# Kernel optimization log

Measured on AMD Instinct MI355X. Metric: run time of the kernel, lower is better.

## Reference

```python
import jax, jax.numpy as jnp
import numpy as np

BATCH = 2048
TEMP = 0.5

def setup_inputs() -> dict:
    key = jax.random.key(0)
    k1, k2 = jax.random.split(key)
    z1 = jax.random.normal(k1, (BATCH, 1024), dtype=jnp.float32)
    z2 = jax.random.normal(k2, (BATCH, 1024), dtype=jnp.float32)
    return {"z1": z1, "z2": z2}

def _l2norm(x, eps=1e-12):
    # matches F.normalize(dim=1): x / max(||x||, eps)
    n = jnp.sqrt(jnp.sum(x * x, axis=1, keepdims=True))
    return x / jnp.maximum(n, eps)

def reference(z1, z2):
    B = z1.shape[0]
    z1n = _l2norm(z1)
    z2n = _l2norm(z2)
    z = jnp.concatenate([z1n, z2n], axis=0)  # [2B, C], unit-norm rows
    # cosine_similarity of unit vectors == dot product -> single GEMM
    S = z @ z.T  # [2B, 2B]
    # positives: S[i, i+B] for i<B and S[i, i-B] for i>=B
    pos_upper = jnp.diagonal(S, offset=B)   # [B]
    pos_lower = jnp.diagonal(S, offset=-B)  # [B]
    positives = jnp.concatenate([pos_upper, pos_lower], axis=0)  # [2B]
    neg_mask = 1.0 - jnp.eye(2 * B, dtype=S.dtype)
    den = jnp.sum(neg_mask * jnp.exp(S / TEMP), axis=1)  # [2B]
    loss = -jnp.mean(positives / TEMP - jnp.log(den))
    return loss
```

## Files before the change

### kernel.cpp

```cpp
#include <hip/hip_runtime.h>
#include <hip/hip_bf16.h>

#define NROW 4096
#define HALFB 2048
#define CDIM 1024
#define INV_T 2.0f
#define NBLK 32
#define NTRI 528
#define NT 8
#define RB 512
#define SCALE_E8M0 122

typedef __attribute__((ext_vector_type(4))) float f32x4;
typedef __attribute__((ext_vector_type(8))) int i32x8;

__device__ __forceinline__ unsigned enc_fp4(float q) {
    const unsigned s = q < 0.f ? 8u : 0u;
    const float a = fabsf(q);
    unsigned m;
    if (a < 1.25f) {
        if (a < 0.25f)      m = 0;
        else if (a < 0.75f) m = 1;
        else                m = 2;
    } else if (a < 2.5f) {
        m = (a < 1.75f) ? 3u : 4u;
    } else {
        if (a < 3.5f)       m = 5;
        else if (a < 5.0f)  m = 6;
        else                m = 7;
    }
    return s | m;
}

__global__ __launch_bounds__(256) void normalize_kernel(
        const float* __restrict__ z1, const float* __restrict__ z2,
        unsigned short* __restrict__ zb4, float* __restrict__ den,
        float* __restrict__ out) {
    const int row = blockIdx.x;
    const int t = threadIdx.x;
    if (row < 16) den[row * 256 + t] = 0.f;
    else if (row == 16 && t == 0) out[0] = 0.f;
    const float* src = (row < HALFB) ? (z1 + (size_t)row * CDIM)
                                     : (z2 + (size_t)(row - HALFB) * CDIM);
    float4 v = ((const float4*)src)[t];
    float ss = v.x * v.x + v.y * v.y + v.z * v.z + v.w * v.w;
    #pragma unroll
    for (int off = 1; off < 64; off <<= 1) ss += __shfl_xor(ss, off);
    __shared__ float wsum[4];
    const int lane = t & 63, wv = t >> 6;
    if (lane == 0) wsum[wv] = ss;
    __syncthreads();
    const float tot = wsum[0] + wsum[1] + wsum[2] + wsum[3];
    const float scale = 32.0f / fmaxf(sqrtf(tot), 1e-12f);
    const unsigned c0 = enc_fp4(v.x * scale);
    const unsigned c1 = enc_fp4(v.y * scale);
    const unsigned c2 = enc_fp4(v.z * scale);
    const unsigned c3 = enc_fp4(v.w * scale);
    zb4[(size_t)row * 256 + t] = (unsigned short)(c0 | (c1 << 4) | (c2 << 8) | (c3 << 12));
}

__global__ __launch_bounds__(256) void gemm_den_kernel(
        const unsigned char* __restrict__ zb4, float* __restrict__ den,
        float* __restrict__ pos) {
    __shared__ __align__(16) unsigned char As[2][128 * 64];
    __shared__ __align__(16) unsigned char Bs[2][128 * 64];

    const int orig = blockIdx.x;
    int swz = (orig & 7) * (NTRI / 8) + (orig >> 3);
    int bi = 0, rem = swz;
    while (rem >= NBLK - bi) { rem -= NBLK - bi; ++bi; }
    const int bj = bi + rem;
    const int i0 = bi * 128, j0 = bj * 128;
    const bool diag = (bi == bj);
    const bool is_pos = (bj == bi + 16);

    const int tid = threadIdx.x;
    const int wave = tid >> 6, lane = tid & 63;
    const int wr = wave >> 1, wc = wave & 1;

    f32x4 acc[4][4];
    #pragma unroll
    for (int m = 0; m < 4; m++)
        #pragma unroll
        for (int n = 0; n < 4; n++) acc[m][n] = (f32x4){0.f, 0.f, 0.f, 0.f};

    const int srow = lane >> 2;
    const int schunk = (lane & 3) ^ ((srow >> 1) & 3);

    const int l15 = lane & 15, ks = lane >> 4;

    auto stage = [&](int buf, int t) {
        const int kb = t * 64;
        #pragma unroll
        for (int c = 0; c < 2; ++c) {
            const int r0 = wave * 32 + c * 16;
            const unsigned char* ga =
                zb4 + (size_t)(i0 + r0 + srow) * RB + kb + schunk * 16;
            __builtin_amdgcn_global_load_lds(
                (const __attribute__((address_space(1))) void*)ga,
                (__attribute__((address_space(3))) void*)(As[buf] + r0 * 64),
                16, 0, 0);
            const unsigned char* gb =
                zb4 + (size_t)(j0 + r0 + srow) * RB + kb + schunk * 16;
            __builtin_amdgcn_global_load_lds(
                (const __attribute__((address_space(1))) void*)gb,
                (__attribute__((address_space(3))) void*)(Bs[buf] + r0 * 64),
                16, 0, 0);
        }
    };

    stage(0, 0);
    asm volatile("s_waitcnt vmcnt(0)" ::: "memory");
    __builtin_amdgcn_s_barrier();

    #pragma unroll
    for (int t = 0; t < NT; ++t) {
        const int buf = t & 1;
        if (t + 1 < NT) stage(buf ^ 1, t + 1);

        i32x8 b[4];
        #pragma unroll
        for (int n = 0; n < 4; ++n) {
            const int r = wc * 64 + n * 16 + l15;
            const int slot = ks ^ ((r >> 1) & 3);
            const int4 w = *(const int4*)(Bs[buf] + r * 64 + slot * 16);
            b[n] = (i32x8){w.x, w.y, w.z, w.w, 0, 0, 0, 0};
        }
        __builtin_amdgcn_s_setprio(1);
        #pragma unroll
        for (int m = 0; m < 4; ++m) {
            const int r = wr * 64 + m * 16 + l15;
            const int slot = ks ^ ((r >> 1) & 3);
            const int4 w = *(const int4*)(As[buf] + r * 64 + slot * 16);
            const i32x8 a = (i32x8){w.x, w.y, w.z, w.w, 0, 0, 0, 0};
            #pragma unroll
            for (int n = 0; n < 4; ++n)
                acc[m][n] = __builtin_amdgcn_mfma_scale_f32_16x16x128_f8f6f4(
                    a, b[n], acc[m][n],
                    4 , 4 ,
                    0, SCALE_E8M0, 0, SCALE_E8M0);
        }
        __builtin_amdgcn_s_setprio(0);
        if (t + 1 < NT) {
            asm volatile("s_waitcnt vmcnt(0)" ::: "memory");
            __builtin_amdgcn_s_barrier();
        }
    }

    if (is_pos && wr == wc) {
        #pragma unroll
        for (int m = 0; m < 4; ++m) {
            #pragma unroll
            for (int r = 0; r < 4; ++r) {
                if (l15 == ks * 4 + r)
                    pos[i0 + wr * 64 + m * 16 + l15] = acc[m][m][r];
            }
        }
    }

    float cs[4] = {0.f, 0.f, 0.f, 0.f};
    #pragma unroll
    for (int m = 0; m < 4; ++m) {
        #pragma unroll
        for (int r = 0; r < 4; ++r) {
            float rs = 0.f;
            #pragma unroll
            for (int n = 0; n < 4; ++n) {
                const float e = __expf(INV_T * acc[m][n][r]);
                rs += e;
                cs[n] += e;
            }
            rs += __shfl_xor(rs, 1);
            rs += __shfl_xor(rs, 2);
            rs += __shfl_xor(rs, 4);
            rs += __shfl_xor(rs, 8);
            if (l15 == 0) {
                const int grow = i0 + wr * 64 + m * 16 + ks * 4 + r;
                atomicAdd(&den[grow], rs);
            }
        }
    }
    if (!diag) {
        #pragma unroll
        for (int n = 0; n < 4; ++n) {
            float c = cs[n];
            c += __shfl_xor(c, 16);
            c += __shfl_xor(c, 32);
            if (lane < 16) {
                const int gcol = j0 + wc * 64 + n * 16 + lane;
                atomicAdd(&den[gcol], c);
            }
        }
    }
}

__global__ __launch_bounds__(256) void loss_kernel(
        const float* __restrict__ den, const float* __restrict__ pos,
        float* __restrict__ out) {
    const float E2 = 7.3890560989306495f;
    const int tid = threadIdx.x;
    const int i = blockIdx.x * 256 + tid;
    float acc = INV_T * pos[i & (HALFB - 1)] - logf(den[i] - E2);
    #pragma unroll
    for (int off = 1; off < 64; off <<= 1) acc += __shfl_xor(acc, off);
    __shared__ float wsum[4];
    const int lane = tid & 63, wv = tid >> 6;
    if (lane == 0) wsum[wv] = acc;
    __syncthreads();
    if (tid == 0)
        atomicAdd(out, -(wsum[0] + wsum[1] + wsum[2] + wsum[3]) * (1.0f / NROW));
}

extern "C" void kernel_launch(void* const* d_in, const int* in_sizes, int n_in,
                              void* d_out, int out_size, void* d_ws, size_t ws_size,
                              hipStream_t stream) {
    const float* z1 = (const float*)d_in[0];
    const float* z2 = (const float*)d_in[1];
    float* out = (float*)d_out;

    unsigned short* zb4 = (unsigned short*)d_ws;
    float* den = (float*)((char*)d_ws + (size_t)NROW * RB);
    float* pos = den + NROW;

    normalize_kernel<<<NROW, 256, 0, stream>>>(z1, z2, zb4, den, out);
    gemm_den_kernel<<<NTRI, 256, 0, stream>>>((const unsigned char*)zb4, den, pos);
    loss_kernel<<<NROW / 256, 256, 0, stream>>>(den, pos, out);
}
```

Measured before the change: 29.49 us.

## Use single-wave 64x64 GEMM tiles and one-wave-per-row normalization

After: 40.61 us. 37.7% more time.

```diff
diff --git a/kernel.cpp b/kernel.cpp
--- a/kernel.cpp
+++ b/kernel.cpp
@@ -5,8 +5,8 @@
 #define HALFB 2048
 #define CDIM 1024
 #define INV_T 2.0f
-#define NBLK 32
-#define NTRI 528
+#define NB64 64
+#define NTRI64 2080
 #define NT 8
 #define RB 512
 #define SCALE_E8M0 122
@@ -36,47 +36,51 @@
         const float* __restrict__ z1, const float* __restrict__ z2,
         unsigned short* __restrict__ zb4, float* __restrict__ den,
         float* __restrict__ out) {
-    const int row = blockIdx.x;
     const int t = threadIdx.x;
-    if (row < 16) den[row * 256 + t] = 0.f;
-    else if (row == 16 && t == 0) out[0] = 0.f;
+    const int wave = t >> 6, lane = t & 63;
+    const int b = blockIdx.x;
+    const int row = b * 4 + wave;
+    if (b < 16) den[b * 256 + t] = 0.f;
+    else if (b == 16 && t == 0) out[0] = 0.f;
     const float* src = (row < HALFB) ? (z1 + (size_t)row * CDIM)
                                      : (z2 + (size_t)(row - HALFB) * CDIM);
-    float4 v = ((const float4*)src)[t];
-    float ss = v.x * v.x + v.y * v.y + v.z * v.z + v.w * v.w;
+    float4 v[4];
+    float ss = 0.f;
+    #pragma unroll
+    for (int p = 0; p < 4; ++p) {
+        v[p] = ((const float4*)src)[p * 64 + lane];
+        ss += v[p].x * v[p].x + v[p].y * v[p].y + v[p].z * v[p].z + v[p].w * v[p].w;
+    }
     #pragma unroll
     for (int off = 1; off < 64; off <<= 1) ss += __shfl_xor(ss, off);
-    __shared__ float wsum[4];
-    const int lane = t & 63, wv = t >> 6;
-    if (lane == 0) wsum[wv] = ss;
-    __syncthreads();
-    const float tot = wsum[0] + wsum[1] + wsum[2] + wsum[3];
-    const float scale = 32.0f / fmaxf(sqrtf(tot), 1e-12f);
-    const unsigned c0 = enc_fp4(v.x * scale);
-    const unsigned c1 = enc_fp4(v.y * scale);
-    const unsigned c2 = enc_fp4(v.z * scale);
-    const unsigned c3 = enc_fp4(v.w * scale);
-    zb4[(size_t)row * 256 + t] = (unsigned short)(c0 | (c1 << 4) | (c2 << 8) | (c3 << 12));
-}
-
-__global__ __launch_bounds__(256) void gemm_den_kernel(
+    const float scale = 32.0f / fmaxf(sqrtf(ss), 1e-12f);
+    #pragma unroll
+    for (int p = 0; p < 4; ++p) {
+        const unsigned c0 = enc_fp4(v[p].x * scale);
+        const unsigned c1 = enc_fp4(v[p].y * scale);
+        const unsigned c2 = enc_fp4(v[p].z * scale);
+        const unsigned c3 = enc_fp4(v[p].w * scale);
+        zb4[(size_t)row * 256 + p * 64 + lane] =
+            (unsigned short)(c0 | (c1 << 4) | (c2 << 8) | (c3 << 12));
+    }
+}
+
+__global__ __launch_bounds__(64) void gemm_den_kernel(
         const unsigned char* __restrict__ zb4, float* __restrict__ den,
         float* __restrict__ pos) {
-    __shared__ __align__(16) unsigned char As[2][128 * 64];
-    __shared__ __align__(16) unsigned char Bs[2][128 * 64];
+    __shared__ __align__(16) unsigned char As[2][64 * 64];
+    __shared__ __align__(16) unsigned char Bs[2][64 * 64];
 
     const int orig = blockIdx.x;
-    int swz = (orig & 7) * (NTRI / 8) + (orig >> 3);
+    int swz = (orig & 7) * (NTRI64 / 8) + (orig >> 3);
     int bi = 0, rem = swz;
-    while (rem >= NBLK - bi) { rem -= NBLK - bi; ++bi; }
+    while (rem >= NB64 - bi) { rem -= NB64 - bi; ++bi; }
     const int bj = bi + rem;
-    const int i0 = bi * 128, j0 = bj * 128;
+    const int i0 = bi * 64, j0 = bj * 64;
     const bool diag = (bi == bj);
-    const bool is_pos = (bj == bi + 16);
-
-    const int tid = threadIdx.x;
-    const int wave = tid >> 6, lane = tid & 63;
-    const int wr = wave >> 1, wc = wave & 1;
+    const bool is_pos = (bj == bi + 32);
+
+    const int lane = threadIdx.x;
 
     f32x4 acc[4][4];
     #pragma unroll
@@ -92,8 +96,8 @@
     auto stage = [&](int buf, int t) {
         const int kb = t * 64;
         #pragma unroll
-        for (int c = 0; c < 2; ++c) {
-            const int r0 = wave * 32 + c * 16;
+        for (int c = 0; c < 4; ++c) {
+            const int r0 = c * 16;
             const unsigned char* ga =
                 zb4 + (size_t)(i0 + r0 + srow) * RB + kb + schunk * 16;
             __builtin_amdgcn_global_load_lds(
@@ -110,18 +114,21 @@
     };
 
     stage(0, 0);
-    asm volatile("s_waitcnt vmcnt(0)" ::: "memory");
-    __builtin_amdgcn_s_barrier();
 
     #pragma unroll
     for (int t = 0; t < NT; ++t) {
         const int buf = t & 1;
-        if (t + 1 < NT) stage(buf ^ 1, t + 1);
+        if (t + 1 < NT) {
+            stage(buf ^ 1, t + 1);
+            asm volatile("s_waitcnt vmcnt(8)" ::: "memory");
+        } else {
+            asm volatile("s_waitcnt vmcnt(0)" ::: "memory");
+        }
 
         i32x8 b[4];
         #pragma unroll
         for (int n = 0; n < 4; ++n) {
-            const int r = wc * 64 + n * 16 + l15;
+            const int r = n * 16 + l15;
             const int slot = ks ^ ((r >> 1) & 3);
             const int4 w = *(const int4*)(Bs[buf] + r * 64 + slot * 16);
             b[n] = (i32x8){w.x, w.y, w.z, w.w, 0, 0, 0, 0};
@@ -129,7 +136,7 @@
         __builtin_amdgcn_s_setprio(1);
         #pragma unroll
         for (int m = 0; m < 4; ++m) {
-            const int r = wr * 64 + m * 16 + l15;
+            const int r = m * 16 + l15;
             const int slot = ks ^ ((r >> 1) & 3);
             const int4 w = *(const int4*)(As[buf] + r * 64 + slot * 16);
             const i32x8 a = (i32x8){w.x, w.y, w.z, w.w, 0, 0, 0, 0};
@@ -141,19 +148,15 @@
                     0, SCALE_E8M0, 0, SCALE_E8M0);
         }
         __builtin_amdgcn_s_setprio(0);
-        if (t + 1 < NT) {
-            asm volatile("s_waitcnt vmcnt(0)" ::: "memory");
-            __builtin_amdgcn_s_barrier();
-        }
-    }
-
-    if (is_pos && wr == wc) {
+    }
+
+    if (is_pos) {
         #pragma unroll
         for (int m = 0; m < 4; ++m) {
             #pragma unroll
             for (int r = 0; r < 4; ++r) {
                 if (l15 == ks * 4 + r)
-                    pos[i0 + wr * 64 + m * 16 + l15] = acc[m][m][r];
+                    pos[i0 + m * 16 + l15] = acc[m][m][r];
             }
         }
     }
@@ -175,7 +178,7 @@
             rs += __shfl_xor(rs, 4);
             rs += __shfl_xor(rs, 8);
             if (l15 == 0) {
-                const int grow = i0 + wr * 64 + m * 16 + ks * 4 + r;
+                const int grow = i0 + m * 16 + ks * 4 + r;
                 atomicAdd(&den[grow], rs);
             }
         }
@@ -187,7 +190,7 @@
             c += __shfl_xor(c, 16);
             c += __shfl_xor(c, 32);
             if (lane < 16) {
-                const int gcol = j0 + wc * 64 + n * 16 + lane;
+                const int gcol = j0 + n * 16 + lane;
                 atomicAdd(&den[gcol], c);
             }
         }
@@ -222,7 +225,7 @@
     float* den = (float*)((char*)d_ws + (size_t)NROW * RB);
     float* pos = den + NROW;
 
-    normalize_kernel<<<NROW, 256, 0, stream>>>(z1, z2, zb4, den, out);
-    gemm_den_kernel<<<NTRI, 256, 0, stream>>>((const unsigned char*)zb4, den, pos);
+    normalize_kernel<<<NROW / 4, 256, 0, stream>>>(z1, z2, zb4, den, out);
+    gemm_den_kernel<<<NTRI64, 64, 0, stream>>>((const unsigned char*)zb4, den, pos);
     loss_kernel<<<NROW / 256, 256, 0, stream>>>(den, pos, out);
 }
```
